# Kernel tuning notes

Hardware: AMD Instinct MI355X
Metric: run time of the kernel (lower is better)

Reference implementation:

```python
import jax, jax.numpy as jnp
import numpy as np

N_NODES = 100000


def gcn_conv(x, edge_index, W, b):
    """PyG-style GCNConv: linear transform, add self-loops, symmetric deg
    normalization, scatter-add aggregation, bias."""
    N = x.shape[0]
    h = x @ W  # [N, out]
    loops = jnp.arange(N, dtype=edge_index.dtype)
    src = jnp.concatenate([edge_index[0], loops])  # message sources (x_j)
    dst = jnp.concatenate([edge_index[1], loops])  # aggregation targets
    ones = jnp.ones(src.shape[0], dtype=h.dtype)
    deg = jax.ops.segment_sum(ones, dst, num_segments=N)
    dinv = jnp.where(deg > 0, jax.lax.rsqrt(deg), 0.0)
    norm = dinv[src] * dinv[dst]  # [E+N]
    msgs = h[src] * norm[:, None]  # gather + scale
    out = jax.ops.segment_sum(msgs, dst, num_segments=N)  # scatter-add
    return out + b


def setup_inputs() -> dict:
    key = jax.random.key(0)
    k1, k2, k3, k4, k5 = jax.random.split(key, 5)
    N, E, D, H = N_NODES, 3200000, 16, 16
    x = jax.random.normal(k1, (N, D), dtype=jnp.float32)
    edge_index = jax.random.randint(k2, (2, E), 0, N, dtype=jnp.int64)
    W1 = jax.random.normal(k3, (D, H), dtype=jnp.float32) / np.sqrt(D)
    b1 = jnp.zeros((H,), dtype=jnp.float32)
    W2 = jax.random.normal(k4, (H, 1), dtype=jnp.float32) / np.sqrt(H)
    b2 = jnp.zeros((1,), dtype=jnp.float32)
    return {"x": x, "edge_index": edge_index, "W1": W1, "b1": b1, "W2": W2, "b2": b2}


def reference(x, edge_index, W1, b1, W2, b2):
    h = jax.nn.relu(gcn_conv(x, edge_index, W1, b1))
    out = gcn_conv(h, edge_index, W2, b2)
    return jnp.squeeze(out, axis=-1)  # [N]
```

## Files before the change

kernel.cpp:

```cpp
#include <hip/hip_runtime.h>
#include <hip/hip_fp16.h>
#include <stdint.h>

#define TPB 256
#define TPBP 512
#define TPBR 1024
#define NPB 256
#define LOG_NPB 8
#define MAXBINS 400
#define NCHUNK 512
#define CHUNK_CAP 6400
#define PCAP 48
#define PB2CAP 8960
#define START_MASK 0x1FFFFFFu

__global__ __launch_bounds__(TPBP) void k_place(const int* __restrict__ ei, int E,
                                                int chunkE, int nbins,
                                                int* __restrict__ baseT,
                                                uint32_t* __restrict__ part) {
    __shared__ uint32_t stage[CHUNK_CAP];
    __shared__ int sstart[MAXBINS];
    __shared__ int scnt[MAXBINS];
    __shared__ int scur[MAXBINS];
    int c = blockIdx.x, t = threadIdx.x;
    int es = c * chunkE, ee = min(E, es + chunkE), n = ee - es;
    for (int i = t; i < nbins; i += TPBP) scur[i] = 0;
    __syncthreads();
    const int* srcs = ei + es;
    const int* dsts = ei + E + es;
    int nv = n >> 2;
    bool al = ((((uintptr_t)srcs) | ((uintptr_t)dsts)) & 15) == 0;
    int4 sb[4], db[4];
    if (al) {
        const int4* s4 = (const int4*)srcs;
        const int4* d4 = (const int4*)dsts;
#pragma unroll
        for (int j = 0; j < 4; ++j) {
            int i = t + j * TPBP;
            if (i < nv) { sb[j] = s4[i]; db[j] = d4[i]; }
        }
#pragma unroll
        for (int j = 0; j < 4; ++j) {
            int i = t + j * TPBP;
            if (i < nv) {
                atomicAdd(&scur[db[j].x >> LOG_NPB], 1);
                atomicAdd(&scur[db[j].y >> LOG_NPB], 1);
                atomicAdd(&scur[db[j].z >> LOG_NPB], 1);
                atomicAdd(&scur[db[j].w >> LOG_NPB], 1);
            }
        }
        for (int i = 4 * nv + t; i < n; i += TPBP)
            atomicAdd(&scur[dsts[i] >> LOG_NPB], 1);
    } else {
        for (int i = t; i < n; i += TPBP)
            atomicAdd(&scur[dsts[i] >> LOG_NPB], 1);
    }
    __syncthreads();
    int val = (t < nbins) ? scur[t] : 0;
    __syncthreads();
    for (int off = 1; off < TPBP; off <<= 1) {
        int add = 0;
        if (t < nbins && t >= off) add = scur[t - off];
        __syncthreads();
        if (t < nbins) scur[t] += add;
        __syncthreads();
    }
    if (t < nbins) {
        sstart[t] = scur[t] - val;
        scnt[t] = val;
        baseT[(size_t)c * nbins + t] = val;
    }
    __syncthreads();
    if (t < nbins) scur[t] = sstart[t];
    __syncthreads();
    if (al) {
#pragma unroll
        for (int j = 0; j < 4; ++j) {
            int i = t + j * TPBP;
            if (i < nv) {
                int slot;
                slot = atomicAdd(&scur[db[j].x >> LOG_NPB], 1);
                stage[slot] = ((uint32_t)sb[j].x << LOG_NPB) | (uint32_t)(db[j].x & (NPB - 1));
                slot = atomicAdd(&scur[db[j].y >> LOG_NPB], 1);
                stage[slot] = ((uint32_t)sb[j].y << LOG_NPB) | (uint32_t)(db[j].y & (NPB - 1));
                slot = atomicAdd(&scur[db[j].z >> LOG_NPB], 1);
                stage[slot] = ((uint32_t)sb[j].z << LOG_NPB) | (uint32_t)(db[j].z & (NPB - 1));
                slot = atomicAdd(&scur[db[j].w >> LOG_NPB], 1);
                stage[slot] = ((uint32_t)sb[j].w << LOG_NPB) | (uint32_t)(db[j].w & (NPB - 1));
            }
        }
        for (int i = 4 * nv + t; i < n; i += TPBP) {
            int s = srcs[i], d = dsts[i];
            int slot = atomicAdd(&scur[d >> LOG_NPB], 1);
            stage[slot] = ((uint32_t)s << LOG_NPB) | (uint32_t)(d & (NPB - 1));
        }
    } else {
        for (int i = t; i < n; i += TPBP) {
            int s = srcs[i], d = dsts[i];
            int slot = atomicAdd(&scur[d >> LOG_NPB], 1);
            stage[slot] = ((uint32_t)s << LOG_NPB) | (uint32_t)(d & (NPB - 1));
        }
    }
    __syncthreads();
    int q = t >> 4, l = t & 15;
    for (int b = q; b < nbins; b += (TPBP >> 4)) {
        int l0 = sstart[b];
        int len = min(scnt[b], PCAP);
        size_t g0 = (size_t)b * ((size_t)NCHUNK * PCAP) + (size_t)c * PCAP;
        for (int i = l; i < len; i += 16)
            part[g0 + i] = stage[l0 + i];
    }
}

__global__ __launch_bounds__(TPBR) void k_rows(const uint32_t* __restrict__ part,
                                               const int* __restrict__ baseT,
                                               const float* __restrict__ x,
                                               const float* __restrict__ W1,
                                               uint32_t* __restrict__ rowInfo,
                                               float* __restrict__ dinv,
                                               int* __restrict__ part2,
                                               __half* __restrict__ g1h,
                                               int N, int nbins) {
    __shared__ uint32_t stageIn[PB2CAP];
    __shared__ uint32_t stageOut[PB2CAP];
    __shared__ int scnt[NCHUNK];
    __shared__ int soff[NCHUNK];
    __shared__ int cnt[NPB];
    __shared__ int cur[NPB];
    int b = blockIdx.x, t = threadIdx.x;
    if (t < NPB) cnt[t] = 0;
    if (t < NCHUNK) {
        int v = min(baseT[(size_t)t * nbins + b], PCAP);
        scnt[t] = v;
        soff[t] = v;
    }
    __syncthreads();
    for (int off = 1; off < NCHUNK; off <<= 1) {
        int add = 0;
        if (t < NCHUNK && t >= off) add = soff[t - off];
        __syncthreads();
        if (t < NCHUNK) soff[t] += add;
        __syncthreads();
    }
    int total = min(soff[NCHUNK - 1], PB2CAP);
    int ex = (t < NCHUNK) ? (soff[t] - scnt[t]) : 0;
    __syncthreads();
    if (t < NCHUNK) soff[t] = ex;
    __syncthreads();
    {
        int g = t >> 4, l = t & 15;
        for (int s = g; s < NCHUNK; s += (TPBR >> 4)) {
            int c2 = scnt[s];
            int base = 4 * l;
            if (l < 12 && base < c2) {
                const uint32_t* seg = part + (size_t)b * ((size_t)NCHUNK * PCAP)
                                           + (size_t)s * PCAP;
                uint4 v = *(const uint4*)(seg + base);
                int o = soff[s] + base;
                int m = min(4, c2 - base);
                uint32_t vv[4] = {v.x, v.y, v.z, v.w};
#pragma unroll
                for (int k = 0; k < 4; ++k) {
                    if (k < m && o + k < PB2CAP) {
                        stageIn[o + k] = vv[k];
                        atomicAdd(&cnt[vv[k] & (NPB - 1)], 1);
                    }
                }
            }
        }
    }
    __syncthreads();
    if (t < NPB) cur[t] = cnt[t];
    __syncthreads();
    for (int off = 1; off < NPB; off <<= 1) {
        int add = 0;
        if (t < NPB && t >= off) add = cur[t - off];
        __syncthreads();
        if (t < NPB) cur[t] += add;
        __syncthreads();
    }
    int deg = (t < NPB) ? cnt[t] : 0;
    int node = b * NPB + (t & (NPB - 1));
    float dv = rsqrtf(1.0f + (float)deg);
    if (t < NPB) {
        int excl = cur[t] - deg;
        if (node < N) {
            uint32_t dg = (uint32_t)min(deg, 127);
            rowInfo[node] = ((uint32_t)(b * PB2CAP + excl) & START_MASK) | (dg << 25);
            dinv[node] = dv;
        }
    }
    __syncthreads();
    if (t < NPB) cur[t] -= cnt[t];
    __syncthreads();
    for (int i = t; i < total; i += TPBR) {
        uint32_t v = stageIn[i];
        int slot = atomicAdd(&cur[v & (NPB - 1)], 1);
        if (slot < PB2CAP) stageOut[slot] = v >> LOG_NPB;
    }
    __syncthreads();
    int* p2 = part2 + (size_t)b * PB2CAP;
    for (int i = t; i < total; i += TPBR) p2[i] = (int)stageOut[i];
    if (t < NPB && node < N) {
        const float4* xv = (const float4*)(x + (size_t)node * 16);
        float4 a = xv[0], bb = xv[1], cc = xv[2], dd = xv[3];
        float xi[16] = {a.x, a.y, a.z, a.w, bb.x, bb.y, bb.z, bb.w,
                        cc.x, cc.y, cc.z, cc.w, dd.x, dd.y, dd.z, dd.w};
        __half2 hp[8];
#pragma unroll
        for (int j = 0; j < 8; ++j) {
            float o0 = 0.f, o1 = 0.f;
#pragma unroll
            for (int k = 0; k < 16; ++k) {
                o0 += xi[k] * W1[k * 16 + 2 * j];
                o1 += xi[k] * W1[k * 16 + 2 * j + 1];
            }
            hp[j] = __floats2half2_rn(o0 * dv, o1 * dv);
        }
        uint4* dst = (uint4*)(g1h + (size_t)node * 16);
        dst[0] = *(uint4*)&hp[0];
        dst[1] = *(uint4*)&hp[4];
    }
}

__global__ __launch_bounds__(256) void k_agg1_csr(const int* __restrict__ part2,
                                                  const uint32_t* __restrict__ rowInfo,
                                                  const __half* __restrict__ g1h,
                                                  const float* __restrict__ dinv,
                                                  const float* __restrict__ b1,
                                                  const float* __restrict__ W2,
                                                  float* __restrict__ g2, int N) {
    int g = threadIdx.x >> 4;
    int l = threadIdx.x & 15;
    int sub = l >> 2;
    int j   = l & 3;
    int n = blockIdx.x * 16 + g;
    if (n >= N) return;
    uint32_t info = rowInfo[n];
    int e0 = (int)(info & START_MASK);
    int e1 = e0 + (int)(info >> 25);
    float a0 = 0.f, a1 = 0.f, a2 = 0.f, a3 = 0.f;
    int e = e0 + sub;
    for (; e + 4 < e1; e += 8) {
        int s0 = part2[e];
        int s1 = part2[e + 4];
        uint2 u0 = *(const uint2*)(g1h + (size_t)s0 * 16 + 4 * j);
        uint2 u1 = *(const uint2*)(g1h + (size_t)s1 * 16 + 4 * j);
        float2 f;
        f = __half22float2(*(__half2*)&u0.x); a0 += f.x; a1 += f.y;
        f = __half22float2(*(__half2*)&u0.y); a2 += f.x; a3 += f.y;
        f = __half22float2(*(__half2*)&u1.x); a0 += f.x; a1 += f.y;
        f = __half22float2(*(__half2*)&u1.y); a2 += f.x; a3 += f.y;
    }
    for (; e < e1; e += 4) {
        int s0 = part2[e];
        uint2 u0 = *(const uint2*)(g1h + (size_t)s0 * 16 + 4 * j);
        float2 f;
        f = __half22float2(*(__half2*)&u0.x); a0 += f.x; a1 += f.y;
        f = __half22float2(*(__half2*)&u0.y); a2 += f.x; a3 += f.y;
    }
    a0 += __shfl_xor(a0, 4); a1 += __shfl_xor(a1, 4);
    a2 += __shfl_xor(a2, 4); a3 += __shfl_xor(a3, 4);
    a0 += __shfl_xor(a0, 8); a1 += __shfl_xor(a1, 8);
    a2 += __shfl_xor(a2, 8); a3 += __shfl_xor(a3, 8);
    {
        uint2 us = *(const uint2*)(g1h + (size_t)n * 16 + 4 * j);
        float2 f;
        f = __half22float2(*(__half2*)&us.x); a0 += f.x; a1 += f.y;
        f = __half22float2(*(__half2*)&us.y); a2 += f.x; a3 += f.y;
    }
    float di = dinv[n];
    float4 b1v = ((const float4*)b1)[j];
    float4 w2v = ((const float4*)W2)[j];
    float p = fmaxf(fmaf(a0, di, b1v.x), 0.f) * w2v.x
            + fmaxf(fmaf(a1, di, b1v.y), 0.f) * w2v.y
            + fmaxf(fmaf(a2, di, b1v.z), 0.f) * w2v.z
            + fmaxf(fmaf(a3, di, b1v.w), 0.f) * w2v.w;
    p += __shfl_xor(p, 1);
    p += __shfl_xor(p, 2);
    if (l == 0) g2[n] = p * di;
}

__global__ __launch_bounds__(256) void k_agg2_csr(const int* __restrict__ part2,
                                                  const uint32_t* __restrict__ rowInfo,
                                                  const float* __restrict__ g2,
                                                  const float* __restrict__ dinv,
                                                  const float* __restrict__ b2,
                                                  float* __restrict__ out, int N) {
    int q = threadIdx.x >> 4, l = threadIdx.x & 15;
    int n = blockIdx.x * 16 + q;
    if (n >= N) return;
    uint32_t info = rowInfo[n];
    int e0 = (int)(info & START_MASK);
    int e1 = e0 + (int)(info >> 25);
    float acc = 0.f;
    for (int e = e0 + l; e < e1; e += 16)
        acc += g2[part2[e]];
    acc += __shfl_xor(acc, 1);
    acc += __shfl_xor(acc, 2);
    acc += __shfl_xor(acc, 4);
    acc += __shfl_xor(acc, 8);
    if (l == 0) out[n] = (acc + g2[n]) * dinv[n] + b2[0];
}

extern "C" void kernel_launch(void* const* d_in, const int* in_sizes, int n_in,
                              void* d_out, int out_size, void* d_ws, size_t ws_size,
                              hipStream_t stream) {
    const float* x  = (const float*)d_in[0];
    const int*   ei = (const int*)d_in[1];
    const float* W1 = (const float*)d_in[2];
    const float* b1 = (const float*)d_in[3];
    const float* W2 = (const float*)d_in[4];
    const float* b2 = (const float*)d_in[5];
    float* out = (float*)d_out;

    const int N = in_sizes[0] / 16;
    const int E = in_sizes[1] / 2;
    const int nbins = (N + NPB - 1) / NPB;
    const int chunkE = (((E + NCHUNK - 1) / NCHUNK) + 15) & ~15;

    float*    dinv    = (float*)d_ws;
    __half*   g1h     = (__half*)(dinv + N);
    uint32_t* part    = (uint32_t*)(g1h + (size_t)16 * N);
    int*      part2   = (int*)(part + (size_t)nbins * NCHUNK * PCAP);
    int*      baseT   = part2 + (size_t)nbins * PB2CAP;
    uint32_t* rowInfo = (uint32_t*)(baseT + (size_t)NCHUNK * nbins);
    float*    g2      = (float*)(rowInfo + N);

    k_place<<<NCHUNK, TPBP, 0, stream>>>(ei, E, chunkE, nbins, baseT, part);
    k_rows<<<nbins, TPBR, 0, stream>>>(part, baseT, x, W1, rowInfo, dinv, part2, g1h, N, nbins);
    k_agg1_csr<<<(N + 15) / 16, TPB, 0, stream>>>(part2, rowInfo, g1h, dinv, b1, W2, g2, N);
    k_agg2_csr<<<(N + 15) / 16, TPB, 0, stream>>>(part2, rowInfo, g2, dinv, b2, out, N);
}
```

Before: 146.6 us.

## Replace per-node CSR build with per-bin LDS atomic aggregation

Drops the second-level sort that built a per-node CSR (part2, rowInfo). Both aggregation passes now read the binned edge partitions directly and accumulate into per-bin shared-memory tables with LDS float atomics. This removes the local counting sort and the CSR write/read traffic, but adds many LDS atomics with possible contention and cuts the grid to one 1024-thread block per 256-node bin (about 391 blocks). W1 is also staged in shared memory.

```diff
diff --git a/kernel.cpp b/kernel.cpp
--- a/kernel.cpp
+++ b/kernel.cpp
@@ -2,17 +2,14 @@
 #include <hip/hip_fp16.h>
 #include <stdint.h>
 
-#define TPB 256
 #define TPBP 512
-#define TPBR 1024
 #define NPB 256
 #define LOG_NPB 8
 #define MAXBINS 400
 #define NCHUNK 512
 #define CHUNK_CAP 6400
 #define PCAP 48
-#define PB2CAP 8960
-#define START_MASK 0x1FFFFFFu
+#define ACCS 17
 
 __global__ __launch_bounds__(TPBP) void k_place(const int* __restrict__ ei, int E,
                                                 int chunkE, int nbins,
@@ -112,96 +109,35 @@
     }
 }
 
-__global__ __launch_bounds__(TPBR) void k_rows(const uint32_t* __restrict__ part,
-                                               const int* __restrict__ baseT,
-                                               const float* __restrict__ x,
-                                               const float* __restrict__ W1,
-                                               uint32_t* __restrict__ rowInfo,
-                                               float* __restrict__ dinv,
-                                               int* __restrict__ part2,
-                                               __half* __restrict__ g1h,
-                                               int N, int nbins) {
-    __shared__ uint32_t stageIn[PB2CAP];
-    __shared__ uint32_t stageOut[PB2CAP];
+__global__ __launch_bounds__(1024) void k_lin(const uint32_t* __restrict__ part,
+                                              const int* __restrict__ baseT,
+                                              const float* __restrict__ x,
+                                              const float* __restrict__ W1,
+                                              float* __restrict__ dinv,
+                                              __half* __restrict__ g1h,
+                                              int N, int nbins) {
     __shared__ int scnt[NCHUNK];
-    __shared__ int soff[NCHUNK];
     __shared__ int cnt[NPB];
-    __shared__ int cur[NPB];
+    __shared__ float sW1[256];
     int b = blockIdx.x, t = threadIdx.x;
     if (t < NPB) cnt[t] = 0;
-    if (t < NCHUNK) {
-        int v = min(baseT[(size_t)t * nbins + b], PCAP);
-        scnt[t] = v;
-        soff[t] = v;
-    }
-    __syncthreads();
-    for (int off = 1; off < NCHUNK; off <<= 1) {
-        int add = 0;
-        if (t < NCHUNK && t >= off) add = soff[t - off];
-        __syncthreads();
-        if (t < NCHUNK) soff[t] += add;
-        __syncthreads();
-    }
-    int total = min(soff[NCHUNK - 1], PB2CAP);
-    int ex = (t < NCHUNK) ? (soff[t] - scnt[t]) : 0;
-    __syncthreads();
-    if (t < NCHUNK) soff[t] = ex;
-    __syncthreads();
-    {
-        int g = t >> 4, l = t & 15;
-        for (int s = g; s < NCHUNK; s += (TPBR >> 4)) {
-            int c2 = scnt[s];
-            int base = 4 * l;
-            if (l < 12 && base < c2) {
-                const uint32_t* seg = part + (size_t)b * ((size_t)NCHUNK * PCAP)
-                                           + (size_t)s * PCAP;
-                uint4 v = *(const uint4*)(seg + base);
-                int o = soff[s] + base;
-                int m = min(4, c2 - base);
-                uint32_t vv[4] = {v.x, v.y, v.z, v.w};
-#pragma unroll
-                for (int k = 0; k < 4; ++k) {
-                    if (k < m && o + k < PB2CAP) {
-                        stageIn[o + k] = vv[k];
-                        atomicAdd(&cnt[vv[k] & (NPB - 1)], 1);
-                    }
-                }
-            }
-        }
-    }
-    __syncthreads();
-    if (t < NPB) cur[t] = cnt[t];
-    __syncthreads();
-    for (int off = 1; off < NPB; off <<= 1) {
-        int add = 0;
-        if (t < NPB && t >= off) add = cur[t - off];
-        __syncthreads();
-        if (t < NPB) cur[t] += add;
-        __syncthreads();
-    }
-    int deg = (t < NPB) ? cnt[t] : 0;
-    int node = b * NPB + (t & (NPB - 1));
-    float dv = rsqrtf(1.0f + (float)deg);
-    if (t < NPB) {
-        int excl = cur[t] - deg;
-        if (node < N) {
-            uint32_t dg = (uint32_t)min(deg, 127);
-            rowInfo[node] = ((uint32_t)(b * PB2CAP + excl) & START_MASK) | (dg << 25);
-            dinv[node] = dv;
-        }
-    }
-    __syncthreads();
-    if (t < NPB) cur[t] -= cnt[t];
-    __syncthreads();
-    for (int i = t; i < total; i += TPBR) {
-        uint32_t v = stageIn[i];
-        int slot = atomicAdd(&cur[v & (NPB - 1)], 1);
-        if (slot < PB2CAP) stageOut[slot] = v >> LOG_NPB;
-    }
-    __syncthreads();
-    int* p2 = part2 + (size_t)b * PB2CAP;
-    for (int i = t; i < total; i += TPBR) p2[i] = (int)stageOut[i];
+    if (t < 256) sW1[t] = W1[t];
+    if (t < NCHUNK) scnt[t] = min(baseT[(size_t)t * nbins + b], PCAP);
+    __syncthreads();
+    const uint32_t* binbase = part + (size_t)b * ((size_t)NCHUNK * PCAP);
+    int w = t >> 6, lane = t & 63;
+    for (int s = w; s < NCHUNK; s += 16) {
+        int c2 = scnt[s];
+        if (lane < c2) {
+            uint32_t v = binbase[(size_t)s * PCAP + lane];
+            atomicAdd(&cnt[v & (NPB - 1)], 1);
+        }
+    }
+    __syncthreads();
+    int node = b * NPB + t;
     if (t < NPB && node < N) {
+        float dv = rsqrtf(1.0f + (float)cnt[t]);
+        dinv[node] = dv;
         const float4* xv = (const float4*)(x + (size_t)node * 16);
         float4 a = xv[0], bb = xv[1], cc = xv[2], dd = xv[3];
         float xi[16] = {a.x, a.y, a.z, a.w, bb.x, bb.y, bb.z, bb.w,
@@ -212,8 +148,8 @@
             float o0 = 0.f, o1 = 0.f;
 #pragma unroll
             for (int k = 0; k < 16; ++k) {
-                o0 += xi[k] * W1[k * 16 + 2 * j];
-                o1 += xi[k] * W1[k * 16 + 2 * j + 1];
+                o0 += xi[k] * sW1[k * 16 + 2 * j];
+                o1 += xi[k] * sW1[k * 16 + 2 * j + 1];
             }
             hp[j] = __floats2half2_rn(o0 * dv, o1 * dv);
         }
@@ -223,84 +159,93 @@
     }
 }
 
-__global__ __launch_bounds__(256) void k_agg1_csr(const int* __restrict__ part2,
-                                                  const uint32_t* __restrict__ rowInfo,
-                                                  const __half* __restrict__ g1h,
-                                                  const float* __restrict__ dinv,
-                                                  const float* __restrict__ b1,
-                                                  const float* __restrict__ W2,
-                                                  float* __restrict__ g2, int N) {
-    int g = threadIdx.x >> 4;
-    int l = threadIdx.x & 15;
-    int sub = l >> 2;
-    int j   = l & 3;
-    int n = blockIdx.x * 16 + g;
-    if (n >= N) return;
-    uint32_t info = rowInfo[n];
-    int e0 = (int)(info & START_MASK);
-    int e1 = e0 + (int)(info >> 25);
-    float a0 = 0.f, a1 = 0.f, a2 = 0.f, a3 = 0.f;
-    int e = e0 + sub;
-    for (; e + 4 < e1; e += 8) {
-        int s0 = part2[e];
-        int s1 = part2[e + 4];
-        uint2 u0 = *(const uint2*)(g1h + (size_t)s0 * 16 + 4 * j);
-        uint2 u1 = *(const uint2*)(g1h + (size_t)s1 * 16 + 4 * j);
-        float2 f;
-        f = __half22float2(*(__half2*)&u0.x); a0 += f.x; a1 += f.y;
-        f = __half22float2(*(__half2*)&u0.y); a2 += f.x; a3 += f.y;
-        f = __half22float2(*(__half2*)&u1.x); a0 += f.x; a1 += f.y;
-        f = __half22float2(*(__half2*)&u1.y); a2 += f.x; a3 += f.y;
-    }
-    for (; e < e1; e += 4) {
-        int s0 = part2[e];
-        uint2 u0 = *(const uint2*)(g1h + (size_t)s0 * 16 + 4 * j);
-        float2 f;
-        f = __half22float2(*(__half2*)&u0.x); a0 += f.x; a1 += f.y;
-        f = __half22float2(*(__half2*)&u0.y); a2 += f.x; a3 += f.y;
-    }
-    a0 += __shfl_xor(a0, 4); a1 += __shfl_xor(a1, 4);
-    a2 += __shfl_xor(a2, 4); a3 += __shfl_xor(a3, 4);
-    a0 += __shfl_xor(a0, 8); a1 += __shfl_xor(a1, 8);
-    a2 += __shfl_xor(a2, 8); a3 += __shfl_xor(a3, 8);
+__global__ __launch_bounds__(1024, 8) void k_agg1b(const uint32_t* __restrict__ part,
+                                                   const int* __restrict__ baseT,
+                                                   const __half* __restrict__ g1h,
+                                                   const float* __restrict__ dinv,
+                                                   const float* __restrict__ b1,
+                                                   const float* __restrict__ W2,
+                                                   float* __restrict__ g2,
+                                                   int N, int nbins) {
+    __shared__ int scnt[NCHUNK];
+    __shared__ float acc[NPB * ACCS];
+    int b = blockIdx.x, t = threadIdx.x;
+    if (t < NCHUNK) scnt[t] = min(baseT[(size_t)t * nbins + b], PCAP);
     {
-        uint2 us = *(const uint2*)(g1h + (size_t)n * 16 + 4 * j);
-        float2 f;
-        f = __half22float2(*(__half2*)&us.x); a0 += f.x; a1 += f.y;
-        f = __half22float2(*(__half2*)&us.y); a2 += f.x; a3 += f.y;
-    }
-    float di = dinv[n];
-    float4 b1v = ((const float4*)b1)[j];
-    float4 w2v = ((const float4*)W2)[j];
-    float p = fmaxf(fmaf(a0, di, b1v.x), 0.f) * w2v.x
-            + fmaxf(fmaf(a1, di, b1v.y), 0.f) * w2v.y
-            + fmaxf(fmaf(a2, di, b1v.z), 0.f) * w2v.z
-            + fmaxf(fmaf(a3, di, b1v.w), 0.f) * w2v.w;
-    p += __shfl_xor(p, 1);
-    p += __shfl_xor(p, 2);
-    if (l == 0) g2[n] = p * di;
-}
-
-__global__ __launch_bounds__(256) void k_agg2_csr(const int* __restrict__ part2,
-                                                  const uint32_t* __restrict__ rowInfo,
-                                                  const float* __restrict__ g2,
-                                                  const float* __restrict__ dinv,
-                                                  const float* __restrict__ b2,
-                                                  float* __restrict__ out, int N) {
-    int q = threadIdx.x >> 4, l = threadIdx.x & 15;
-    int n = blockIdx.x * 16 + q;
-    if (n >= N) return;
-    uint32_t info = rowInfo[n];
-    int e0 = (int)(info & START_MASK);
-    int e1 = e0 + (int)(info >> 25);
-    float acc = 0.f;
-    for (int e = e0 + l; e < e1; e += 16)
-        acc += g2[part2[e]];
-    acc += __shfl_xor(acc, 1);
-    acc += __shfl_xor(acc, 2);
-    acc += __shfl_xor(acc, 4);
-    acc += __shfl_xor(acc, 8);
-    if (l == 0) out[n] = (acc + g2[n]) * dinv[n] + b2[0];
+        int n2 = t >> 2, k = t & 3;
+        int node = b * NPB + n2;
+        float4 f = make_float4(0.f, 0.f, 0.f, 0.f);
+        if (node < N) {
+            uint2 u = *(const uint2*)(g1h + (size_t)node * 16 + 4 * k);
+            float2 f0 = __half22float2(*(__half2*)&u.x);
+            float2 f1 = __half22float2(*(__half2*)&u.y);
+            f = make_float4(f0.x, f0.y, f1.x, f1.y);
+        }
+        int base = n2 * ACCS + 4 * k;
+        acc[base + 0] = f.x; acc[base + 1] = f.y;
+        acc[base + 2] = f.z; acc[base + 3] = f.w;
+    }
+    __syncthreads();
+    const uint32_t* binbase = part + (size_t)b * ((size_t)NCHUNK * PCAP);
+    int w = t >> 6, lane = t & 63;
+    int team = lane >> 2, k = lane & 3;
+    for (int s = w; s < NCHUNK; s += 16) {
+        int c2 = scnt[s];
+        const uint32_t* seg = binbase + (size_t)s * PCAP;
+        for (int e = team; e < c2; e += 16) {
+            uint32_t v = seg[e];
+            int src = (int)(v >> LOG_NPB);
+            int dl = (int)(v & (NPB - 1));
+            uint2 u = *(const uint2*)(g1h + (size_t)src * 16 + 4 * k);
+            float2 f0 = __half22float2(*(__half2*)&u.x);
+            float2 f1 = __half22float2(*(__half2*)&u.y);
+            int base = dl * ACCS + 4 * k;
+            atomicAdd(&acc[base + 0], f0.x);
+            atomicAdd(&acc[base + 1], f0.y);
+            atomicAdd(&acc[base + 2], f1.x);
+            atomicAdd(&acc[base + 3], f1.y);
+        }
+    }
+    __syncthreads();
+    int node = b * NPB + t;
+    if (t < NPB && node < N) {
+        float di = dinv[node];
+        float p = 0.f;
+#pragma unroll
+        for (int j = 0; j < 16; ++j) {
+            float h = fmaf(acc[t * ACCS + j], di, b1[j]);
+            p += fmaxf(h, 0.f) * W2[j];
+        }
+        g2[node] = p * di;
+    }
+}
+
+__global__ __launch_bounds__(1024) void k_agg2b(const uint32_t* __restrict__ part,
+                                                const int* __restrict__ baseT,
+                                                const float* __restrict__ g2,
+                                                const float* __restrict__ dinv,
+                                                const float* __restrict__ b2,
+                                                float* __restrict__ out,
+                                                int N, int nbins) {
+    __shared__ int scnt[NCHUNK];
+    __shared__ float acc2[NPB];
+    int b = blockIdx.x, t = threadIdx.x;
+    if (t < NPB) acc2[t] = 0.f;
+    if (t < NCHUNK) scnt[t] = min(baseT[(size_t)t * nbins + b], PCAP);
+    __syncthreads();
+    const uint32_t* binbase = part + (size_t)b * ((size_t)NCHUNK * PCAP);
+    int w = t >> 6, lane = t & 63;
+    for (int s = w; s < NCHUNK; s += 16) {
+        int c2 = scnt[s];
+        if (lane < c2) {
+            uint32_t v = binbase[(size_t)s * PCAP + lane];
+            atomicAdd(&acc2[v & (NPB - 1)], g2[v >> LOG_NPB]);
+        }
+    }
+    __syncthreads();
+    int node = b * NPB + t;
+    if (t < NPB && node < N)
+        out[node] = fmaf(acc2[t] + g2[node], dinv[node], b2[0]);
 }
 
 extern "C" void kernel_launch(void* const* d_in, const int* in_sizes, int n_in,
@@ -319,16 +264,14 @@
     const int nbins = (N + NPB - 1) / NPB;
     const int chunkE = (((E + NCHUNK - 1) / NCHUNK) + 15) & ~15;
 
-    float*    dinv    = (float*)d_ws;
-    __half*   g1h     = (__half*)(dinv + N);
-    uint32_t* part    = (uint32_t*)(g1h + (size_t)16 * N);
-    int*      part2   = (int*)(part + (size_t)nbins * NCHUNK * PCAP);
-    int*      baseT   = part2 + (size_t)nbins * PB2CAP;
-    uint32_t* rowInfo = (uint32_t*)(baseT + (size_t)NCHUNK * nbins);
-    float*    g2      = (float*)(rowInfo + N);
+    float*    dinv  = (float*)d_ws;
+    __half*   g1h   = (__half*)(dinv + N);
+    uint32_t* part  = (uint32_t*)(g1h + (size_t)16 * N);
+    int*      baseT = (int*)(part + (size_t)nbins * NCHUNK * PCAP);
+    float*    g2    = (float*)(baseT + (size_t)NCHUNK * nbins);
 
     k_place<<<NCHUNK, TPBP, 0, stream>>>(ei, E, chunkE, nbins, baseT, part);
-    k_rows<<<nbins, TPBR, 0, stream>>>(part, baseT, x, W1, rowInfo, dinv, part2, g1h, N, nbins);
-    k_agg1_csr<<<(N + 15) / 16, TPB, 0, stream>>>(part2, rowInfo, g1h, dinv, b1, W2, g2, N);
-    k_agg2_csr<<<(N + 15) / 16, TPB, 0, stream>>>(part2, rowInfo, g2, dinv, b2, out, N);
-}
+    k_lin<<<nbins, 1024, 0, stream>>>(part, baseT, x, W1, dinv, g1h, N, nbins);
+    k_agg1b<<<nbins, 1024, 0, stream>>>(part, baseT, g1h, dinv, b1, W2, g2, N, nbins);
+    k_agg2b<<<nbins, 1024, 0, stream>>>(part, baseT, g2, dinv, b2, out, N, nbins);
+}
```

After: 477.5 us. 226% more time.
